# Kernel optimization log

Hardware: AMD Instinct MI355X
Metric: run time of the kernel (lower is better)

The kernel has to match this reference:

```python
import jax, jax.numpy as jnp
import numpy as np

D_MODEL = 1024
H = 16
DK = D_MODEL // H


def setup_inputs() -> dict:
    key = jax.random.key(0)
    ks = jax.random.split(key, 13)
    B, S = 2, 2048
    scale = 1.0 / np.sqrt(D_MODEL)
    inp = {
        "query": jax.random.normal(ks[0], (B, S, D_MODEL), jnp.float32),
        "key": jax.random.normal(ks[1], (B, S, D_MODEL), jnp.float32),
        "value": jax.random.normal(ks[2], (B, S, D_MODEL), jnp.float32),
        "mask": jax.random.randint(ks[3], (B, 1, S, S), 0, 2, jnp.int32),
        "Wq": jax.random.normal(ks[4], (D_MODEL, D_MODEL), jnp.float32) * scale,
        "bq": jnp.zeros((D_MODEL,), jnp.float32),
        "Wk": jax.random.normal(ks[5], (D_MODEL, D_MODEL), jnp.float32) * scale,
        "bk": jnp.zeros((D_MODEL,), jnp.float32),
        "Wv": jax.random.normal(ks[6], (D_MODEL, D_MODEL), jnp.float32) * scale,
        "bv": jnp.zeros((D_MODEL,), jnp.float32),
        "Wo": jax.random.normal(ks[7], (D_MODEL, D_MODEL), jnp.float32) * scale,
        "bo": jnp.zeros((D_MODEL,), jnp.float32),
    }
    return inp


def _split_heads(x, W, b):
    # torch Linear: x @ W.T + b; then [B,S,D] -> [B,H,S,DK]
    B, S, _ = x.shape
    out = x @ W.T + b
    return out.reshape(B, S, H, DK).transpose(0, 2, 1, 3)


def reference(query, key, value, mask, Wq, bq, Wk, bk, Wv, bv, Wo, bo):
    B, S, _ = query.shape
    q = _split_heads(query, Wq, bq)   # [B,H,S,DK]
    k = _split_heads(key, Wk, bk)
    v = _split_heads(value, Wv, bv)
    scores = jnp.einsum("bhqd,bhkd->bhqk", q, k) / jnp.sqrt(jnp.asarray(DK, q.dtype))
    scores = jnp.where(mask == 0, jnp.asarray(-1e9, scores.dtype), scores)
    prob = jax.nn.softmax(scores, axis=-1)
    out = jnp.einsum("bhqk,bhkd->bhqd", prob, v)  # [B,H,S,DK]
    out = out.transpose(0, 2, 1, 3).reshape(B, S, D_MODEL)
    return out @ Wo.T + bo
```

## Files before the change

kernel.cpp:

```cpp
#include <hip/hip_runtime.h>
#include <hip/hip_bf16.h>

#define B_   2
#define S_   2048
#define DM   1024
#define NH   16
#define Mdim 4096
#define Kdim 1024

typedef __attribute__((ext_vector_type(8))) short bf16x8;
typedef __attribute__((ext_vector_type(4))) short bf16x4;
typedef __attribute__((ext_vector_type(4))) float f32x4;

__device__ __forceinline__ short f2b(float x) {
  union { __hip_bfloat16 h; short s; } u;
  u.h = __float2bfloat16(x);
  return u.s;
}

__device__ __forceinline__ size_t blk_idx(int row, int k) {
  return ((size_t)(row >> 7) * 32 + (k >> 5)) * 4096 + (row & 127) * 32 + (k & 31);
}

__device__ __forceinline__ void async_copy16(const void* g, void* l) {
  __builtin_amdgcn_global_load_lds(
      (const __attribute__((address_space(1))) unsigned int*)g,
      (__attribute__((address_space(3))) unsigned int*)l, 16, 0, 0);
}

struct Cvt7 {
  const float* src[7];
  ushort* dst[7];
  int n[7];
};

__global__ __launch_bounds__(256) void cvt_all(Cvt7 c) {
  const int ten = blockIdx.y;
  const int base = (blockIdx.x * 256 + threadIdx.x) * 8;
  if (base >= c.n[ten]) return;
  const float* s = c.src[ten] + base;
  float4 a = *(const float4*)s;
  float4 b = *(const float4*)(s + 4);
  bf16x8 r;
  r[0] = f2b(a.x); r[1] = f2b(a.y); r[2] = f2b(a.z); r[3] = f2b(a.w);
  r[4] = f2b(b.x); r[5] = f2b(b.y); r[6] = f2b(b.z); r[7] = f2b(b.w);
  const int row = base >> 10, k = base & 1023;
  *(bf16x8*)(c.dst[ten] + blk_idx(row, k)) = r;
}

__global__ __launch_bounds__(256) void pack_mask(const int* __restrict__ mask,
                                                 unsigned long long* __restrict__ mpk) {
  const int gw = (blockIdx.x * 256 + threadIdx.x) >> 6;
  const int lane = threadIdx.x & 63;
  const int mv = mask[(size_t)gw * 64 + lane];
  const unsigned long long bits = __ballot(mv != 0);
  if (lane == 0) mpk[gw] = bits;
}

__global__ __launch_bounds__(256) void fill_bias(float* __restrict__ out,
                                                 const float* __restrict__ bias) {
  const int t = blockIdx.x * 256 + threadIdx.x;
  ((float4*)out)[t] = *(const float4*)&bias[(t * 4) & (DM - 1)];
}

struct Proj {
  const ushort* A[3];
  const ushort* W[3];
  const float* bias[3];
  ushort* out[3];
};

__global__ __launch_bounds__(256) void gemm_qkv(Proj p) {
  const int z = blockIdx.z;
  const int t = threadIdx.x;
  const int w = t >> 6, lane = t & 63;
  const int quad = lane >> 4, r16 = lane & 15;
  const int wr = w >> 1, wc = w & 1;
  const int row0 = blockIdx.x * 128, col0 = blockIdx.y * 128;

  __shared__ alignas(16) ushort a_s[2][4096];
  __shared__ alignas(16) ushort b_s[2][4096];

  const ushort* Ab = p.A[z] + (size_t)blockIdx.x * 32 * 4096 + (size_t)t * 8;
  const ushort* Wb = p.W[z] + (size_t)blockIdx.y * 32 * 4096 + (size_t)t * 8;
  const int lo0 = w * 512, lo1 = 2048 + w * 512;

#define STAGE(buf, kb)                                  \
  do {                                                  \
    const size_t off = (size_t)(kb) * 4096;             \
    async_copy16(Ab + off, &a_s[buf][lo0]);             \
    async_copy16(Ab + off + 2048, &a_s[buf][lo1]);      \
    async_copy16(Wb + off, &b_s[buf][lo0]);             \
    async_copy16(Wb + off + 2048, &b_s[buf][lo1]);      \
  } while (0)

  f32x4 acc[4][4];
#pragma unroll
  for (int mt = 0; mt < 4; ++mt)
#pragma unroll
    for (int nt = 0; nt < 4; ++nt) acc[mt][nt] = (f32x4){0.f, 0.f, 0.f, 0.f};

  STAGE(0, 0);
  int cur = 0;
  for (int kb = 0; kb < 32; ++kb) {
    __syncthreads();
    if (kb + 1 < 32) STAGE(1 - cur, kb + 1);
    bf16x8 af[4], bfr[4];
#pragma unroll
    for (int mt = 0; mt < 4; ++mt)
      af[mt] = *(const bf16x8*)&a_s[cur][(wr * 64 + mt * 16 + r16) * 32 + quad * 8];
#pragma unroll
    for (int nt = 0; nt < 4; ++nt)
      bfr[nt] = *(const bf16x8*)&b_s[cur][(wc * 64 + nt * 16 + r16) * 32 + quad * 8];
#pragma unroll
    for (int mt = 0; mt < 4; ++mt)
#pragma unroll
      for (int nt = 0; nt < 4; ++nt)
        acc[mt][nt] = __builtin_amdgcn_mfma_f32_16x16x32_bf16(af[mt], bfr[nt],
                                                              acc[mt][nt], 0, 0, 0);
    cur ^= 1;
  }

  const float scale = (z == 0) ? 0.125f : 1.0f;
  ushort* Cv = p.out[z];
#pragma unroll
  for (int mt = 0; mt < 4; ++mt) {
#pragma unroll
    for (int nt = 0; nt < 4; ++nt) {
      const int col = col0 + wc * 64 + nt * 16 + r16;
      const float bv = p.bias[z][col];
      const int rowb = row0 + wr * 64 + mt * 16 + quad * 4;
#pragma unroll
      for (int i = 0; i < 4; ++i) {
        const float v = (acc[mt][nt][i] + bv) * scale;
        const int row = rowb + i;
        const int bb = row >> 11, s = row & (S_ - 1);
        const int hh = col >> 6, d = col & 63;
        if (z == 0) {
          Cv[(size_t)row * DM + col] = (ushort)f2b(v);
        } else if (z == 1) {
          const size_t idx = ((size_t)(bb * NH + hh) * S_ + s) * 64 +
                             (((d >> 3) ^ (s & 7)) * 8) + (d & 7);
          Cv[idx] = (ushort)f2b(v);
        } else {
          const size_t idx = ((size_t)(bb * NH + hh) * 64 + d) * S_ + (s & ~63) +
                             ((((s >> 3) & 7) ^ (d & 7)) * 8) + (s & 7);
          Cv[idx] = (ushort)f2b(v);
        }
      }
    }
  }
}

__global__ __launch_bounds__(256) void gemm_out(const ushort* __restrict__ A,
                                                const ushort* __restrict__ W,
                                                float* __restrict__ out) {
  const int kz = blockIdx.z;
  const int t = threadIdx.x;
  const int w = t >> 6, lane = t & 63;
  const int quad = lane >> 4, r16 = lane & 15;
  const int wr = w >> 1, wc = w & 1;
  const int row0 = blockIdx.x * 128, col0 = blockIdx.y * 128;

  __shared__ alignas(16) ushort a_s[2][4096];
  __shared__ alignas(16) ushort b_s[2][4096];

  const ushort* Ab = A + (size_t)blockIdx.x * 32 * 4096 + (size_t)t * 8;
  const ushort* Wb = W + (size_t)blockIdx.y * 32 * 4096 + (size_t)t * 8;
  const int lo0 = w * 512, lo1 = 2048 + w * 512;

  f32x4 acc[4][4];
#pragma unroll
  for (int mt = 0; mt < 4; ++mt)
#pragma unroll
    for (int nt = 0; nt < 4; ++nt) acc[mt][nt] = (f32x4){0.f, 0.f, 0.f, 0.f};

  const int kb0 = kz * 16;
  STAGE(0, kb0);
  int cur = 0;
  for (int kb = kb0; kb < kb0 + 16; ++kb) {
    __syncthreads();
    if (kb + 1 < kb0 + 16) STAGE(1 - cur, kb + 1);
    bf16x8 af[4], bfr[4];
#pragma unroll
    for (int mt = 0; mt < 4; ++mt)
      af[mt] = *(const bf16x8*)&a_s[cur][(wr * 64 + mt * 16 + r16) * 32 + quad * 8];
#pragma unroll
    for (int nt = 0; nt < 4; ++nt)
      bfr[nt] = *(const bf16x8*)&b_s[cur][(wc * 64 + nt * 16 + r16) * 32 + quad * 8];
#pragma unroll
    for (int mt = 0; mt < 4; ++mt)
#pragma unroll
      for (int nt = 0; nt < 4; ++nt)
        acc[mt][nt] = __builtin_amdgcn_mfma_f32_16x16x32_bf16(af[mt], bfr[nt],
                                                              acc[mt][nt], 0, 0, 0);
    cur ^= 1;
  }
#undef STAGE

#pragma unroll
  for (int mt = 0; mt < 4; ++mt) {
#pragma unroll
    for (int nt = 0; nt < 4; ++nt) {
      const int col = col0 + wc * 64 + nt * 16 + r16;
      const int rowb = row0 + wr * 64 + mt * 16 + quad * 4;
#pragma unroll
      for (int i = 0; i < 4; ++i)
        unsafeAtomicAdd(&out[(size_t)(rowb + i) * DM + col], acc[mt][nt][i]);
    }
  }
}

__global__ __launch_bounds__(256) void attn_mfma(const ushort* __restrict__ Qp,
                                                 const ushort* __restrict__ Kg,
                                                 const ushort* __restrict__ Vg,
                                                 const unsigned long long* __restrict__ mpk,
                                                 ushort* __restrict__ Oa) {
  const int bh = blockIdx.y;
  const int b = bh >> 4, h = bh & 15;
  const int q0 = blockIdx.x * 64;
  const int t = threadIdx.x;
  const int w = t >> 6, lane = t & 63, quad = lane >> 4, r16 = lane & 15;
  const size_t rb = (size_t)b * S_;

  __shared__ alignas(16) ushort k_s[64 * 64];
  __shared__ alignas(16) ushort vt_s[64 * 64];
  __shared__ alignas(16) ushort p_s[4][16 * 76];

  const ushort* qptr = Qp + (rb + q0 + w * 16 + r16) * DM + h * 64 + quad * 8;
  const bf16x8 aq0 = *(const bf16x8*)qptr;
  const bf16x8 aq1 = *(const bf16x8*)(qptr + 32);

  float l_i[4] = {0.f, 0.f, 0.f, 0.f};
  f32x4 oacc[4];
#pragma unroll
  for (int nt = 0; nt < 4; ++nt) oacc[nt] = (f32x4){0.f, 0.f, 0.f, 0.f};

  const ushort* kgb = Kg + (size_t)bh * S_ * 64 + (size_t)t * 8;
  const ushort* vgb = Vg + (size_t)bh * 64 * S_ + (size_t)(t >> 3) * S_ + (t & 7) * 8;
  ushort* kl0 = &k_s[w * 512];
  ushort* kl1 = &k_s[2048 + w * 512];
  ushort* vl0 = &vt_s[w * 512];
  ushort* vl1 = &vt_s[2048 + w * 512];

  const unsigned long long* mrowp = mpk + (rb + q0 + w * 16 + quad * 4) * 32;

  for (int kt = 0; kt < S_; kt += 64) {
    __syncthreads();
    async_copy16(kgb + (size_t)kt * 64, kl0);
    async_copy16(kgb + (size_t)(kt + 32) * 64, kl1);
    async_copy16(vgb + kt, vl0);
    async_copy16(vgb + (size_t)32 * S_ + kt, vl1);
    __syncthreads();

    f32x4 sacc[4];
#pragma unroll
    for (int nt = 0; nt < 4; ++nt) {
      sacc[nt] = (f32x4){0.f, 0.f, 0.f, 0.f};
      const int krow = nt * 16 + r16;
      const bf16x8 b0 = *(const bf16x8*)&k_s[krow * 64 + ((quad ^ (krow & 7)) * 8)];
      const bf16x8 b1 = *(const bf16x8*)&k_s[krow * 64 + (((4 + quad) ^ (krow & 7)) * 8)];
      sacc[nt] = __builtin_amdgcn_mfma_f32_16x16x32_bf16(aq0, b0, sacc[nt], 0, 0, 0);
      sacc[nt] = __builtin_amdgcn_mfma_f32_16x16x32_bf16(aq1, b1, sacc[nt], 0, 0, 0);
    }

    const int seg = kt >> 6;
#pragma unroll
    for (int i = 0; i < 4; ++i) {
      const unsigned long long mbits = mrowp[i * 32 + seg];
      float ps = 0.f;
#pragma unroll
      for (int nt = 0; nt < 4; ++nt) {
        const unsigned int bit = (unsigned int)(mbits >> (nt * 16 + r16)) & 1u;
        const float p = bit ? __expf(sacc[nt][i]) : 0.f;
        ps += p;
        p_s[w][(quad * 4 + i) * 76 + nt * 16 + r16] = (ushort)f2b(p);
      }
      l_i[i] += ps;
    }

#pragma unroll
    for (int ks = 0; ks < 2; ++ks) {
      const bf16x4 lo = *(const bf16x4*)&p_s[w][r16 * 76 + ks * 32 + quad * 8];
      const bf16x4 hi = *(const bf16x4*)&p_s[w][r16 * 76 + ks * 32 + quad * 8 + 4];
      bf16x8 pa;
#pragma unroll
      for (int j = 0; j < 4; ++j) { pa[j] = lo[j]; pa[4 + j] = hi[j]; }
      const int kc = ks * 4 + quad;
#pragma unroll
      for (int nt = 0; nt < 4; ++nt) {
        const int dk = nt * 16 + r16;
        const bf16x8 vb = *(const bf16x8*)&vt_s[dk * 64 + ((kc ^ (dk & 7)) * 8)];
        oacc[nt] = __builtin_amdgcn_mfma_f32_16x16x32_bf16(pa, vb, oacc[nt], 0, 0, 0);
      }
    }
  }

#pragma unroll
  for (int i = 0; i < 4; ++i) {
    float l = l_i[i];
#pragma unroll
    for (int off = 1; off < 16; off <<= 1) l += __shfl_xor(l, off);
    l_i[i] = l;
  }
#pragma unroll
  for (int nt = 0; nt < 4; ++nt) {
#pragma unroll
    for (int i = 0; i < 4; ++i) {
      const int row = (int)rb + q0 + w * 16 + quad * 4 + i;
      const int col = h * 64 + nt * 16 + r16;
      Oa[blk_idx(row, col)] = (ushort)f2b(oacc[nt][i] / l_i[i]);
    }
  }
}

extern "C" void kernel_launch(void* const* d_in, const int* in_sizes, int n_in,
                              void* d_out, int out_size, void* d_ws, size_t ws_size,
                              hipStream_t stream) {
  const int* mask = (const int*)d_in[3];
  const float* bo = (const float*)d_in[11];

  const size_t NE = (size_t)B_ * S_ * DM;
  const size_t NW = (size_t)DM * DM;

  ushort* qc = (ushort*)d_ws;
  ushort* kc = qc + NE;
  ushort* vc = kc + NE;
  ushort* Qp = vc + NE;
  ushort* Kg = Qp + NE;
  ushort* Vg = Kg + NE;
  ushort* Wqc = Vg + NE;
  ushort* Wkc = Wqc + NW;
  ushort* Wvc = Wkc + NW;
  ushort* Woc = Wvc + NW;
  unsigned long long* mpk = (unsigned long long*)kc;

  Cvt7 c;
  const int sidx[7] = {0, 1, 2, 4, 6, 8, 10};
  ushort* dsts[7] = {qc, kc, vc, Wqc, Wkc, Wvc, Woc};
  for (int i = 0; i < 7; ++i) {
    c.src[i] = (const float*)d_in[sidx[i]];
    c.dst[i] = dsts[i];
    c.n[i] = (i < 3) ? (int)NE : (int)NW;
  }
  cvt_all<<<dim3(2048, 7), 256, 0, stream>>>(c);

  Proj p;
  p.A[0] = qc;  p.A[1] = kc;  p.A[2] = vc;
  p.W[0] = Wqc; p.W[1] = Wkc; p.W[2] = Wvc;
  p.bias[0] = (const float*)d_in[5];
  p.bias[1] = (const float*)d_in[7];
  p.bias[2] = (const float*)d_in[9];
  p.out[0] = Qp; p.out[1] = Kg; p.out[2] = Vg;
  gemm_qkv<<<dim3(Mdim / 128, DM / 128, 3), 256, 0, stream>>>(p);

  pack_mask<<<(B_ * S_ * (S_ / 64) * 64) / 256, 256, 0, stream>>>(mask, mpk);

  attn_mfma<<<dim3(S_ / 64, B_ * NH), 256, 0, stream>>>(Qp, Kg, Vg, mpk, qc);

  fill_bias<<<(int)(NE / 4 / 256), 256, 0, stream>>>((float*)d_out, bo);
  gemm_out<<<dim3(Mdim / 128, DM / 128, 2), 256, 0, stream>>>(qc, Woc, (float*)d_out);
}
```

Before: 310.0 us.

## Compute transposed scores so P stays in registers, dropping LDS round-trip

The attention kernel now computes S^T (K as the A operand, Q as the B operand), so each lane's MFMA output already matches the A-operand layout needed for the P·V MFMA. This removes the per-tile shared-memory write and read of P, and the V store layout in the QKV projection is permuted to match the new key ordering. Mask bits are read once per lane row, and row sums are reduced with fewer shuffles. The conversion kernel also now has each thread write 16 contiguous blocked elements with coalesced stores, launching half as many blocks.

```diff
diff --git a/kernel.cpp b/kernel.cpp
--- a/kernel.cpp
+++ b/kernel.cpp
@@ -9,7 +9,6 @@
 #define Kdim 1024
 
 typedef __attribute__((ext_vector_type(8))) short bf16x8;
-typedef __attribute__((ext_vector_type(4))) short bf16x4;
 typedef __attribute__((ext_vector_type(4))) float f32x4;
 
 __device__ __forceinline__ short f2b(float x) {
@@ -36,16 +35,22 @@
 
 __global__ __launch_bounds__(256) void cvt_all(Cvt7 c) {
   const int ten = blockIdx.y;
-  const int base = (blockIdx.x * 256 + threadIdx.x) * 8;
-  if (base >= c.n[ten]) return;
-  const float* s = c.src[ten] + base;
-  float4 a = *(const float4*)s;
-  float4 b = *(const float4*)(s + 4);
-  bf16x8 r;
-  r[0] = f2b(a.x); r[1] = f2b(a.y); r[2] = f2b(a.z); r[3] = f2b(a.w);
-  r[4] = f2b(b.x); r[5] = f2b(b.y); r[6] = f2b(b.z); r[7] = f2b(b.w);
-  const int row = base >> 10, k = base & 1023;
-  *(bf16x8*)(c.dst[ten] + blk_idx(row, k)) = r;
+  const int tau = blockIdx.x;
+  if (tau >= (c.n[ten] >> 12)) return;
+  const int t = threadIdx.x;
+  const int row = (tau >> 5) * 128 + (t >> 1);
+  const int k = (tau & 31) * 32 + (t & 1) * 16;
+  const float* s = c.src[ten] + (size_t)row * 1024 + k;
+  ushort* d = c.dst[ten] + (size_t)tau * 4096 + t * 16;
+#pragma unroll
+  for (int h = 0; h < 2; ++h) {
+    float4 a = *(const float4*)(s + h * 8);
+    float4 b = *(const float4*)(s + h * 8 + 4);
+    bf16x8 r;
+    r[0] = f2b(a.x); r[1] = f2b(a.y); r[2] = f2b(a.z); r[3] = f2b(a.w);
+    r[4] = f2b(b.x); r[5] = f2b(b.y); r[6] = f2b(b.z); r[7] = f2b(b.w);
+    *(bf16x8*)(d + h * 8) = r;
+  }
 }
 
 __global__ __launch_bounds__(256) void pack_mask(const int* __restrict__ mask,
@@ -69,21 +74,6 @@
   const float* bias[3];
   ushort* out[3];
 };
-
-__global__ __launch_bounds__(256) void gemm_qkv(Proj p) {
-  const int z = blockIdx.z;
-  const int t = threadIdx.x;
-  const int w = t >> 6, lane = t & 63;
-  const int quad = lane >> 4, r16 = lane & 15;
-  const int wr = w >> 1, wc = w & 1;
-  const int row0 = blockIdx.x * 128, col0 = blockIdx.y * 128;
-
-  __shared__ alignas(16) ushort a_s[2][4096];
-  __shared__ alignas(16) ushort b_s[2][4096];
-
-  const ushort* Ab = p.A[z] + (size_t)blockIdx.x * 32 * 4096 + (size_t)t * 8;
-  const ushort* Wb = p.W[z] + (size_t)blockIdx.y * 32 * 4096 + (size_t)t * 8;
-  const int lo0 = w * 512, lo1 = 2048 + w * 512;
 
 #define STAGE(buf, kb)                                  \
   do {                                                  \
@@ -93,6 +83,21 @@
     async_copy16(Wb + off, &b_s[buf][lo0]);             \
     async_copy16(Wb + off + 2048, &b_s[buf][lo1]);      \
   } while (0)
+
+__global__ __launch_bounds__(256) void gemm_qkv(Proj p) {
+  const int z = blockIdx.z;
+  const int t = threadIdx.x;
+  const int w = t >> 6, lane = t & 63;
+  const int quad = lane >> 4, r16 = lane & 15;
+  const int wr = w >> 1, wc = w & 1;
+  const int row0 = blockIdx.x * 128, col0 = blockIdx.y * 128;
+
+  __shared__ alignas(16) ushort a_s[2][4096];
+  __shared__ alignas(16) ushort b_s[2][4096];
+
+  const ushort* Ab = p.A[z] + (size_t)blockIdx.x * 32 * 4096 + (size_t)t * 8;
+  const ushort* Wb = p.W[z] + (size_t)blockIdx.y * 32 * 4096 + (size_t)t * 8;
+  const int lo0 = w * 512, lo1 = 2048 + w * 512;
 
   f32x4 acc[4][4];
 #pragma unroll
@@ -143,8 +148,11 @@
                              (((d >> 3) ^ (s & 7)) * 8) + (d & 7);
           Cv[idx] = (ushort)f2b(v);
         } else {
+          const int s6 = s & 63;
+          const int K16 = s6 >> 4, q4 = (s6 >> 2) & 3, ii = s6 & 3;
+          const int pos = (K16 >> 1) * 32 + q4 * 8 + (K16 & 1) * 4 + ii;
           const size_t idx = ((size_t)(bb * NH + hh) * 64 + d) * S_ + (s & ~63) +
-                             ((((s >> 3) & 7) ^ (d & 7)) * 8) + (s & 7);
+                             (((pos >> 3) ^ (d & 7)) * 8) + (pos & 7);
           Cv[idx] = (ushort)f2b(v);
         }
       }
@@ -225,13 +233,12 @@
 
   __shared__ alignas(16) ushort k_s[64 * 64];
   __shared__ alignas(16) ushort vt_s[64 * 64];
-  __shared__ alignas(16) ushort p_s[4][16 * 76];
 
   const ushort* qptr = Qp + (rb + q0 + w * 16 + r16) * DM + h * 64 + quad * 8;
-  const bf16x8 aq0 = *(const bf16x8*)qptr;
-  const bf16x8 aq1 = *(const bf16x8*)(qptr + 32);
-
-  float l_i[4] = {0.f, 0.f, 0.f, 0.f};
+  const bf16x8 bq0 = *(const bf16x8*)qptr;
+  const bf16x8 bq1 = *(const bf16x8*)(qptr + 32);
+
+  float l_lane = 0.f;
   f32x4 oacc[4];
 #pragma unroll
   for (int nt = 0; nt < 4; ++nt) oacc[nt] = (f32x4){0.f, 0.f, 0.f, 0.f};
@@ -243,7 +250,7 @@
   ushort* vl0 = &vt_s[w * 512];
   ushort* vl1 = &vt_s[2048 + w * 512];
 
-  const unsigned long long* mrowp = mpk + (rb + q0 + w * 16 + quad * 4) * 32;
+  const unsigned long long* mrowp = mpk + (rb + q0 + w * 16 + r16) * 32;
 
   for (int kt = 0; kt < S_; kt += 64) {
     __syncthreads();
@@ -255,61 +262,54 @@
 
     f32x4 sacc[4];
 #pragma unroll
-    for (int nt = 0; nt < 4; ++nt) {
-      sacc[nt] = (f32x4){0.f, 0.f, 0.f, 0.f};
-      const int krow = nt * 16 + r16;
-      const bf16x8 b0 = *(const bf16x8*)&k_s[krow * 64 + ((quad ^ (krow & 7)) * 8)];
-      const bf16x8 b1 = *(const bf16x8*)&k_s[krow * 64 + (((4 + quad) ^ (krow & 7)) * 8)];
-      sacc[nt] = __builtin_amdgcn_mfma_f32_16x16x32_bf16(aq0, b0, sacc[nt], 0, 0, 0);
-      sacc[nt] = __builtin_amdgcn_mfma_f32_16x16x32_bf16(aq1, b1, sacc[nt], 0, 0, 0);
-    }
-
-    const int seg = kt >> 6;
-#pragma unroll
-    for (int i = 0; i < 4; ++i) {
-      const unsigned long long mbits = mrowp[i * 32 + seg];
-      float ps = 0.f;
-#pragma unroll
-      for (int nt = 0; nt < 4; ++nt) {
-        const unsigned int bit = (unsigned int)(mbits >> (nt * 16 + r16)) & 1u;
-        const float p = bit ? __expf(sacc[nt][i]) : 0.f;
-        ps += p;
-        p_s[w][(quad * 4 + i) * 76 + nt * 16 + r16] = (ushort)f2b(p);
+    for (int mt = 0; mt < 4; ++mt) {
+      const int krow = mt * 16 + r16;
+      const bf16x8 a0 = *(const bf16x8*)&k_s[krow * 64 + ((quad ^ (krow & 7)) * 8)];
+      const bf16x8 a1 = *(const bf16x8*)&k_s[krow * 64 + (((4 + quad) ^ (krow & 7)) * 8)];
+      f32x4 z = (f32x4){0.f, 0.f, 0.f, 0.f};
+      z = __builtin_amdgcn_mfma_f32_16x16x32_bf16(a0, bq0, z, 0, 0, 0);
+      sacc[mt] = __builtin_amdgcn_mfma_f32_16x16x32_bf16(a1, bq1, z, 0, 0, 0);
+    }
+
+    const unsigned long long mbits = mrowp[kt >> 6];
+    bf16x8 pa0, pa1;
+#pragma unroll
+    for (int mt = 0; mt < 4; ++mt) {
+#pragma unroll
+      for (int i = 0; i < 4; ++i) {
+        const unsigned int bit =
+            (unsigned int)(mbits >> (mt * 16 + quad * 4 + i)) & 1u;
+        const float p = bit ? __expf(sacc[mt][i]) : 0.f;
+        l_lane += p;
+        const short pb = f2b(p);
+        if (mt < 2) pa0[(mt & 1) * 4 + i] = pb;
+        else        pa1[(mt & 1) * 4 + i] = pb;
       }
-      l_i[i] += ps;
     }
 
 #pragma unroll
     for (int ks = 0; ks < 2; ++ks) {
-      const bf16x4 lo = *(const bf16x4*)&p_s[w][r16 * 76 + ks * 32 + quad * 8];
-      const bf16x4 hi = *(const bf16x4*)&p_s[w][r16 * 76 + ks * 32 + quad * 8 + 4];
-      bf16x8 pa;
-#pragma unroll
-      for (int j = 0; j < 4; ++j) { pa[j] = lo[j]; pa[4 + j] = hi[j]; }
-      const int kc = ks * 4 + quad;
+      const bf16x8 pa = ks ? pa1 : pa0;
 #pragma unroll
       for (int nt = 0; nt < 4; ++nt) {
         const int dk = nt * 16 + r16;
-        const bf16x8 vb = *(const bf16x8*)&vt_s[dk * 64 + ((kc ^ (dk & 7)) * 8)];
+        const bf16x8 vb =
+            *(const bf16x8*)&vt_s[dk * 64 + (((ks * 4 + quad) ^ (dk & 7)) * 8)];
         oacc[nt] = __builtin_amdgcn_mfma_f32_16x16x32_bf16(pa, vb, oacc[nt], 0, 0, 0);
       }
     }
   }
 
+  l_lane += __shfl_xor(l_lane, 16);
+  l_lane += __shfl_xor(l_lane, 32);
 #pragma unroll
   for (int i = 0; i < 4; ++i) {
-    float l = l_i[i];
-#pragma unroll
-    for (int off = 1; off < 16; off <<= 1) l += __shfl_xor(l, off);
-    l_i[i] = l;
-  }
-#pragma unroll
-  for (int nt = 0; nt < 4; ++nt) {
-#pragma unroll
-    for (int i = 0; i < 4; ++i) {
-      const int row = (int)rb + q0 + w * 16 + quad * 4 + i;
+    const float lq = __shfl(l_lane, quad * 4 + i);
+    const int row = (int)rb + q0 + w * 16 + quad * 4 + i;
+#pragma unroll
+    for (int nt = 0; nt < 4; ++nt) {
       const int col = h * 64 + nt * 16 + r16;
-      Oa[blk_idx(row, col)] = (ushort)f2b(oacc[nt][i] / l_i[i]);
+      Oa[blk_idx(row, col)] = (ushort)f2b(oacc[nt][i] / lq);
     }
   }
 }
@@ -343,7 +343,7 @@
     c.dst[i] = dsts[i];
     c.n[i] = (i < 3) ? (int)NE : (int)NW;
   }
-  cvt_all<<<dim3(2048, 7), 256, 0, stream>>>(c);
+  cvt_all<<<dim3(1024, 7), 256, 0, stream>>>(c);
 
   Proj p;
   p.A[0] = qc;  p.A[1] = kc;  p.A[2] = vc;
```

Measured after the change: 307.4 us. Within noise of the previous version (-0.9%).
